# Kernel tuning notes

Hardware: AMD Instinct MI355X
Metric: run time of the kernel (lower is better)

Reference implementation:

```python
import jax, jax.numpy as jnp
import numpy as np
from jax import lax

_CLIP_MIN = 1e-06
_CLIP_MAX = 1.0
_POS_ALPHA = 0.0005
NUM_CLASSES = 21
RADIUS = 3
HALF_D = RADIUS * RADIUS
POOL = 3
PAD = POOL // 2
IGNORE = 255
LAM = 0.5  # loss_weight_lambda, lambda_way=1


def _max_pool(x):
    # NCHW max pool, kernel=stride=3, padding=1
    return lax.reduce_window(x, -jnp.inf, lax.max,
                             (1, 1, POOL, POOL), (1, 1, POOL, POOL),
                             ((0, 0), (0, 0), (PAD, PAD), (PAD, PAD)))


def _get_pairs(x):
    # stack radius*radius shifted crops -> [N, C, r^2, nh, nw]
    h, w = x.shape[2], x.shape[3]
    nh, nw = h - RADIUS + 1, w - RADIUS + 1
    crops = [x[:, :, y:y + nh, xo:xo + nw] for y in range(RADIUS) for xo in range(RADIUS)]
    return jnp.stack(crops, axis=2)


def _log_det_by_cholesky(m):
    chol = jnp.linalg.cholesky(m)
    return 2.0 * jnp.sum(jnp.log(jnp.diagonal(chol, axis1=-2, axis2=-1) + 1e-08), axis=-1)


def _rmi_lower_bound(labels_4d, probs_4d):
    la = _max_pool(labels_4d)
    pr = _max_pool(probs_4d)
    n, c = la.shape[0], la.shape[1]
    la_v = _get_pairs(la).reshape(n, c, HALF_D, -1)   # [N,C,d,L]
    pr_v = _get_pairs(pr).reshape(n, c, HALF_D, -1)
    la_v = la_v - jnp.mean(la_v, axis=3, keepdims=True)
    pr_v = pr_v - jnp.mean(pr_v, axis=3, keepdims=True)
    la_cov = jnp.einsum('ncdl,ncel->ncde', la_v, la_v)
    pr_cov = jnp.einsum('ncdl,ncel->ncde', pr_v, pr_v)
    eye = jnp.eye(HALF_D, dtype=la_cov.dtype)
    pr_cov_inv = jnp.linalg.inv(pr_cov + eye * _POS_ALPHA)
    la_pr_cov = jnp.einsum('ncdl,ncel->ncde', la_v, pr_v)
    appro_var = la_cov - jnp.einsum('ncde,ncef,ncgf->ncdg', la_pr_cov, pr_cov_inv, la_pr_cov)
    rmi_now = 0.5 * _log_det_by_cholesky(appro_var + eye * _POS_ALPHA)  # [N,C]
    rmi_per_class = jnp.mean(rmi_now.reshape(-1, NUM_CLASSES), axis=0) / float(HALF_D)
    return jnp.sum(rmi_per_class)


def setup_inputs() -> dict:
    key = jax.random.key(0)
    k1, k2 = jax.random.split(key)
    score = jax.random.normal(k1, (4, NUM_CLASSES, 512, 512), dtype=jnp.float32)
    target = jax.random.randint(k2, (4, 512, 512), 0, NUM_CLASSES, dtype=jnp.int64)
    return {"score": score, "target": target}


def reference(score, target):
    # cross entropy with ignore_index=255, mean reduction
    logp = jax.nn.log_softmax(score, axis=1)                      # [N,C,H,W]
    valid_ce = (target != IGNORE)
    safe_t = jnp.where(valid_ce, target, 0)
    nll = -jnp.take_along_axis(logp, safe_t[:, None].astype(jnp.int32), axis=1)[:, 0]
    normal_loss = jnp.sum(jnp.where(valid_ce, nll, 0.0)) / jnp.sum(valid_ce.astype(jnp.float32))

    # valid one-hot labels and masked sigmoid probs
    mask = (target < NUM_CLASSES)                                 # [N,H,W]
    maskf = mask.astype(jnp.float32)
    onehot = jax.nn.one_hot((target * mask).astype(jnp.int32), NUM_CLASSES, dtype=jnp.float32)
    onehot = onehot * maskf[..., None]                            # [N,H,W,C]
    onehot = jnp.transpose(onehot, (0, 3, 1, 2))                  # [N,C,H,W]
    probs = jnp.clip(jax.nn.sigmoid(score) * maskf[:, None], _CLIP_MIN, _CLIP_MAX)

    rmi_loss = _rmi_lower_bound(onehot, probs)
    return LAM * normal_loss + rmi_loss * (1.0 - LAM)
```

## Files before the change

kernel.cpp:

```cpp
#include <hip/hip_runtime.h>
#include <cfloat>
#include <cmath>

#define DEVINL __device__ __forceinline__

constexpr int N_ = 4, C_ = 21, H_ = 512, W_ = 512;
constexpr int P_ = 171;
constexpr int Q_ = 169;
constexpr int NC_ = N_ * C_;
constexpr int HW_ = H_ * W_;
constexpr int PP_ = P_ * P_;
constexpr int PROW_ = 172;
constexpr int PPAD_ = PROW_ * P_;
constexpr int NCOV_ = 189;
constexpr float EPS_ = 5e-4f;
constexpr int RC_ = 29;
constexpr int G_ = 43;

DEVINL constexpr int tstart(int d) { return d * 9 - d * (d - 1) / 2; }

DEVINL float wave_sum(float v) {
#pragma unroll
    for (int o = 32; o > 0; o >>= 1) v += __shfl_down(v, o, 64);
    return v;
}

__global__ __launch_bounds__(256) void k_bits(const int* __restrict__ target,
                                              unsigned* __restrict__ pack) {
    int tid = blockIdx.x * 256 + threadIdx.x;
    if (tid >= N_ * PP_) return;
    int cell = tid % PP_;
    int n = tid / PP_;
    int j = cell % P_;
    int i = cell / P_;
    int hl = 3 * i - 1; if (hl < 0) hl = 0;
    int wl = 3 * j - 1; if (wl < 0) wl = 0;
    int hmax = 3 * i + 1, wmax = 3 * j + 1;
    const int* tb = target + (size_t)n * HW_;
    unsigned oh = 0, px = 0;
#pragma unroll
    for (int r = 0; r < 3; ++r) {
        int hh = hl + r;
        bool hv = hh <= hmax;
        const int* trow = tb + hh * W_;
#pragma unroll
        for (int dc = 0; dc < 3; ++dc) {
            int ww = wl + dc;
            int t = trow[ww];
            if (hv && (ww <= wmax) && t >= 0 && t < C_) {
                oh |= 1u << t;
                px |= 1u << (r * 3 + dc);
            }
        }
    }
    pack[tid] = oh | (px << 23);
}

__global__ __launch_bounds__(256) void k_ce(const float* __restrict__ score,
                                            const int* __restrict__ target,
                                            float* __restrict__ cov_ce) {
    int tid = blockIdx.x * 256 + threadIdx.x;
    int p0 = tid * 4;
    int n = p0 >> 18;
    int hw = p0 & (HW_ - 1);
    const float* sp = score + (size_t)n * C_ * HW_ + hw;

    float4 s[C_];
#pragma unroll
    for (int c = 0; c < C_; ++c)
        s[c] = *(const float4*)(sp + (size_t)c * HW_);
    int4 t4 = *(const int4*)(target + p0);

    float4 se = {0.f, 0.f, 0.f, 0.f};
    float4 stgt = {0.f, 0.f, 0.f, 0.f};
#pragma unroll
    for (int c = 0; c < C_; ++c) {
        se.x += __expf(s[c].x);
        se.y += __expf(s[c].y);
        se.z += __expf(s[c].z);
        se.w += __expf(s[c].w);
        if (t4.x == c) stgt.x = s[c].x;
        if (t4.y == c) stgt.y = s[c].y;
        if (t4.z == c) stgt.z = s[c].z;
        if (t4.w == c) stgt.w = s[c].w;
    }
    float nll = 0.f, cnt = 0.f;
    if (t4.x != 255) { nll += __logf(se.x) - stgt.x; cnt += 1.f; }
    if (t4.y != 255) { nll += __logf(se.y) - stgt.y; cnt += 1.f; }
    if (t4.z != 255) { nll += __logf(se.z) - stgt.z; cnt += 1.f; }
    if (t4.w != 255) { nll += __logf(se.w) - stgt.w; cnt += 1.f; }

    nll = wave_sum(nll);
    cnt = wave_sum(cnt);
    __shared__ float rn[4], rc[4];
    int wv = threadIdx.x >> 6, lane = threadIdx.x & 63;
    if (lane == 0) { rn[wv] = nll; rc[wv] = cnt; }
    __syncthreads();
    if (threadIdx.x == 0) {
        atomicAdd(&cov_ce[NC_ * NCOV_ + 0], rn[0] + rn[1] + rn[2] + rn[3]);
        atomicAdd(&cov_ce[NC_ * NCOV_ + 1], rc[0] + rc[1] + rc[2] + rc[3]);
    }
}

template <int IDX>
DEVINL void do_cell(const float (&f)[3][16], unsigned pk, int c, float* prp, float* lap) {
    unsigned px = pk >> 23;
    float vm = -FLT_MAX;
#pragma unroll
    for (int r = 0; r < 3; ++r)
#pragma unroll
        for (int dc = 0; dc < 3; ++dc)
            vm = fmaxf(vm, ((px >> (r * 3 + dc)) & 1u) ? f[r][IDX + dc] : -FLT_MAX);
    float p = __builtin_amdgcn_rcpf(1.f + __expf(-vm));
    p = fminf(fmaxf(p, 1e-6f), 1.f);
    *prp = p;
    *lap = ((pk >> c) & 1u) ? 1.f : 0.f;
}

__global__ __launch_bounds__(256) void k_pool(const float* __restrict__ score,
                                              const unsigned* __restrict__ pack,
                                              float* __restrict__ pr,
                                              float* __restrict__ la) {
    int tid = blockIdx.x * 256 + threadIdx.x;
    if (tid >= NC_ * P_ * G_) return;
    int g = tid % G_;
    int rest = tid / G_;
    int i = rest % P_;
    int ncidx = rest / P_;
    int n = ncidx / C_;
    int c = ncidx - n * C_;

    int hl = 3 * i - 1; if (hl < 0) hl = 0;
    int b = (g == 0) ? 0 : 12 * g - 4;
    int o3 = (b + 15 < W_) ? 12 : 8;

    const float* sb = score + (size_t)ncidx * HW_ + (size_t)hl * W_ + b;
    float f[3][16];
#pragma unroll
    for (int r = 0; r < 3; ++r) {
        const float* rp = sb + r * W_;
        float4 q0 = *(const float4*)(rp);
        float4 q1 = *(const float4*)(rp + 4);
        float4 q2 = *(const float4*)(rp + 8);
        float4 q3 = *(const float4*)(rp + o3);
        f[r][0] = q0.x;  f[r][1] = q0.y;  f[r][2] = q0.z;  f[r][3] = q0.w;
        f[r][4] = q1.x;  f[r][5] = q1.y;  f[r][6] = q1.z;  f[r][7] = q1.w;
        f[r][8] = q2.x;  f[r][9] = q2.y;  f[r][10] = q2.z; f[r][11] = q2.w;
        f[r][12] = q3.x; f[r][13] = q3.y; f[r][14] = q3.z; f[r][15] = q3.w;
    }

    const unsigned* pkp = pack + n * PP_ + i * P_ + 4 * g;
    size_t ob = (size_t)ncidx * PPAD_ + (size_t)i * PROW_ + 4 * g;
    if (g == 0) {
        do_cell<0>(f, pkp[0], c, pr + ob + 0, la + ob + 0);
        do_cell<2>(f, pkp[1], c, pr + ob + 1, la + ob + 1);
        do_cell<5>(f, pkp[2], c, pr + ob + 2, la + ob + 2);
        do_cell<8>(f, pkp[3], c, pr + ob + 3, la + ob + 3);
    } else {
        do_cell<3>(f, pkp[0], c, pr + ob + 0, la + ob + 0);
        do_cell<6>(f, pkp[1], c, pr + ob + 1, la + ob + 1);
        do_cell<9>(f, pkp[2], c, pr + ob + 2, la + ob + 2);
        if (4 * g + 3 < P_)
            do_cell<12>(f, pkp[3], c, pr + ob + 3, la + ob + 3);
    }
}

__global__ __launch_bounds__(256) void k_cov(const float* __restrict__ la,
                                             const float* __restrict__ pr,
                                             float* __restrict__ cov) {
    int nc = blockIdx.x;
    int chunk = blockIdx.y;
    int part = blockIdx.z;
    int r0 = chunk * RC_;
    int rend = r0 + RC_;
    if (rend > Q_) rend = Q_;
    int nitems = (rend - r0) * G_;

    __shared__ float red[4][81];
    int lane = threadIdx.x & 63;
    int wv = threadIdx.x >> 6;

    if (part < 2) {
        const float* X = (part == 0 ? la : pr) + (size_t)nc * PPAD_;
        float s1[9], s2[45];
#pragma unroll
        for (int k = 0; k < 9; ++k) s1[k] = 0.f;
#pragma unroll
        for (int k = 0; k < 45; ++k) s2[k] = 0.f;
        for (int idx = threadIdx.x; idx < nitems; idx += 256) {
            int lr = idx / G_;
            int q = idx - lr * G_;
            int x0 = q * 4;
            const float* base = X + (r0 + lr) * PROW_ + x0;
            float v[3][8];
#pragma unroll
            for (int r = 0; r < 3; ++r) {
                float4 u0 = *(const float4*)(base + r * PROW_);
                float4 u1 = *(const float4*)(base + r * PROW_ + 4);
                v[r][0] = u0.x; v[r][1] = u0.y; v[r][2] = u0.z; v[r][3] = u0.w;
                v[r][4] = u1.x; v[r][5] = u1.y; v[r][6] = u1.z; v[r][7] = u1.w;
            }
#pragma unroll
            for (int p = 0; p < 4; ++p) {
                if (x0 + p < Q_) {
#pragma unroll
                    for (int d = 0; d < 9; ++d) s1[d] += v[d / 3][p + d % 3];
                    int k = 0;
#pragma unroll
                    for (int d = 0; d < 9; ++d)
#pragma unroll
                        for (int e = d; e < 9; ++e) {
                            s2[k] += v[d / 3][p + d % 3] * v[e / 3][p + e % 3];
                            ++k;
                        }
                }
            }
        }
#pragma unroll
        for (int k = 0; k < 9; ++k) { float v2 = wave_sum(s1[k]); if (lane == 0) red[wv][k] = v2; }
#pragma unroll
        for (int k = 0; k < 45; ++k) { float v2 = wave_sum(s2[k]); if (lane == 0) red[wv][9 + k] = v2; }
        __syncthreads();
        int b1 = (part == 0) ? 0 : 9;
        int b2 = (part == 0) ? 18 : 63;
        for (int k = threadIdx.x; k < 54; k += 256) {
            float v2 = red[0][k] + red[1][k] + red[2][k] + red[3][k];
            int dst = (k < 9) ? (b1 + k) : (b2 + k - 9);
            atomicAdd(&cov[nc * NCOV_ + dst], v2);
        }
    } else {
        const float* A = la + (size_t)nc * PPAD_;
        const float* B = pr + (size_t)nc * PPAD_;
        float sab[81];
#pragma unroll
        for (int k = 0; k < 81; ++k) sab[k] = 0.f;
        for (int idx = threadIdx.x; idx < nitems; idx += 256) {
            int lr = idx / G_;
            int q = idx - lr * G_;
            int x0 = q * 4;
            size_t off = (size_t)(r0 + lr) * PROW_ + x0;
            float a[3][8], b[3][8];
#pragma unroll
            for (int r = 0; r < 3; ++r) {
                float4 u0 = *(const float4*)(A + off + r * PROW_);
                float4 u1 = *(const float4*)(A + off + r * PROW_ + 4);
                a[r][0] = u0.x; a[r][1] = u0.y; a[r][2] = u0.z; a[r][3] = u0.w;
                a[r][4] = u1.x; a[r][5] = u1.y; a[r][6] = u1.z; a[r][7] = u1.w;
                float4 w0 = *(const float4*)(B + off + r * PROW_);
                float4 w1 = *(const float4*)(B + off + r * PROW_ + 4);
                b[r][0] = w0.x; b[r][1] = w0.y; b[r][2] = w0.z; b[r][3] = w0.w;
                b[r][4] = w1.x; b[r][5] = w1.y; b[r][6] = w1.z; b[r][7] = w1.w;
            }
#pragma unroll
            for (int p = 0; p < 4; ++p) {
                if (x0 + p < Q_) {
#pragma unroll
                    for (int d = 0; d < 9; ++d)
#pragma unroll
                        for (int e = 0; e < 9; ++e)
                            sab[d * 9 + e] += a[d / 3][p + d % 3] * b[e / 3][p + e % 3];
                }
            }
        }
#pragma unroll
        for (int k = 0; k < 81; ++k) { float v2 = wave_sum(sab[k]); if (lane == 0) red[wv][k] = v2; }
        __syncthreads();
        for (int k = threadIdx.x; k < 81; k += 256) {
            float v2 = red[0][k] + red[1][k] + red[2][k] + red[3][k];
            atomicAdd(&cov[nc * NCOV_ + 108 + k], v2);
        }
    }
}

__global__ __launch_bounds__(128) void k_final(const float* __restrict__ cov,
                                               float* __restrict__ out) {
    __shared__ float red[128];
    int t = threadIdx.x;
    float my = 0.f;
    if (t < NC_) {
        const float* S = cov + t * NCOV_;
        const float Lf = (float)(Q_ * Q_);
        float sA[9], sB[9];
#pragma unroll
        for (int d = 0; d < 9; ++d) { sA[d] = S[d]; sB[d] = S[9 + d]; }
        float laC[45], M[45], Cm[81];
        {
            int k = 0;
#pragma unroll
            for (int d = 0; d < 9; ++d)
#pragma unroll
                for (int e = d; e < 9; ++e) {
                    laC[k] = S[18 + k] - sA[d] * sA[e] / Lf;
                    M[k] = S[63 + k] - sB[d] * sB[e] / Lf + (d == e ? EPS_ : 0.f);
                    ++k;
                }
#pragma unroll
            for (int d = 0; d < 9; ++d)
#pragma unroll
                for (int e = 0; e < 9; ++e)
                    Cm[d * 9 + e] = S[108 + d * 9 + e] - sA[d] * sB[e] / Lf;
        }
#pragma unroll
        for (int j = 0; j < 9; ++j) {
            float s = M[tstart(j)];
#pragma unroll
            for (int k = 0; k < j; ++k) { float l = M[tstart(k) + (j - k)]; s -= l * l; }
            float dj = sqrtf(fmaxf(s, 1e-30f));
            M[tstart(j)] = dj;
            float inv = 1.f / dj;
#pragma unroll
            for (int i = j + 1; i < 9; ++i) {
                float s2 = M[tstart(j) + (i - j)];
#pragma unroll
                for (int k = 0; k < j; ++k)
                    s2 -= M[tstart(k) + (i - k)] * M[tstart(k) + (j - k)];
                M[tstart(j) + (i - j)] = s2 * inv;
            }
        }
#pragma unroll
        for (int p = 0; p < 9; ++p) {
#pragma unroll
            for (int i = 0; i < 9; ++i) {
                float s = Cm[p * 9 + i];
#pragma unroll
                for (int k = 0; k < i; ++k)
                    s -= M[tstart(k) + (i - k)] * Cm[p * 9 + k];
                Cm[p * 9 + i] = s / M[tstart(i)];
            }
        }
#pragma unroll
        for (int d = 0; d < 9; ++d)
#pragma unroll
            for (int e = d; e < 9; ++e) {
                float s = 0.f;
#pragma unroll
                for (int i = 0; i < 9; ++i) s += Cm[d * 9 + i] * Cm[e * 9 + i];
                laC[tstart(d) + (e - d)] -= s;
                if (d == e) laC[tstart(d)] += EPS_;
            }
        float rmi = 0.f;
#pragma unroll
        for (int j = 0; j < 9; ++j) {
            float s = laC[tstart(j)];
#pragma unroll
            for (int k = 0; k < j; ++k) { float l = laC[tstart(k) + (j - k)]; s -= l * l; }
            float dj = sqrtf(fmaxf(s, 0.f));
            laC[tstart(j)] = dj;
            float inv = 1.f / fmaxf(dj, 1e-30f);
#pragma unroll
            for (int i = j + 1; i < 9; ++i) {
                float s2 = laC[tstart(j) + (i - j)];
#pragma unroll
                for (int k = 0; k < j; ++k)
                    s2 -= laC[tstart(k) + (i - k)] * laC[tstart(k) + (j - k)];
                laC[tstart(j) + (i - j)] = s2 * inv;
            }
            rmi += __logf(dj + 1e-8f);
        }
        my = rmi;
    }
    red[t] = my;
    __syncthreads();
#pragma unroll
    for (int o = 64; o > 0; o >>= 1) {
        if (t < o) red[t] += red[t + o];
        __syncthreads();
    }
    if (t == 0) {
        float rmi_total = red[0] / 36.f;
        float ce = cov[NC_ * NCOV_ + 0] / cov[NC_ * NCOV_ + 1];
        out[0] = 0.5f * ce + 0.5f * rmi_total;
    }
}

extern "C" void kernel_launch(void* const* d_in, const int* in_sizes, int n_in,
                              void* d_out, int out_size, void* d_ws, size_t ws_size,
                              hipStream_t stream) {
    const float* score = (const float*)d_in[0];
    const int* target = (const int*)d_in[1];
    float* pr = (float*)d_ws;
    float* la = pr + (size_t)NC_ * PPAD_;
    float* cov = la + (size_t)NC_ * PPAD_;
    unsigned* pack = (unsigned*)(cov + NC_ * NCOV_ + 2);
    hipMemsetAsync(cov, 0, (size_t)(NC_ * NCOV_ + 2) * sizeof(float), stream);

    k_bits<<<dim3((N_ * PP_ + 255) / 256), dim3(256), 0, stream>>>(target, pack);
    k_ce<<<dim3(N_ * HW_ / 4 / 256), dim3(256), 0, stream>>>(score, target, cov);
    k_pool<<<dim3((NC_ * P_ * G_ + 255) / 256), dim3(256), 0, stream>>>(score, pack, pr, la);
    k_cov<<<dim3(NC_, 6, 3), dim3(256), 0, stream>>>(la, pr, cov);
    k_final<<<dim3(1), dim3(128), 0, stream>>>(cov, (float*)d_out);
}
```

Measured before the change: 254.1 us.

## Stage covariance tiles in LDS and split moment terms across waves

The covariance kernel now copies the la and pr row chunks for each (nc, chunk) into shared memory once. Eight waves then each compute a disjoint subset of the self and cross moment terms from LDS, instead of three separate blocks each rereading global memory. Every wave reduces its own accumulators with wave shuffles and issues atomics directly, so the block-level shared reduction is gone. In exchange the grid has fewer blocks, the load is uneven across waves, each wave issues more atomics, and 512-thread blocks use large LDS.

```diff
diff --git a/kernel.cpp b/kernel.cpp
--- a/kernel.cpp
+++ b/kernel.cpp
@@ -9,13 +9,14 @@
 constexpr int Q_ = 169;
 constexpr int NC_ = N_ * C_;
 constexpr int HW_ = H_ * W_;
-constexpr int PP_ = P_ * P_;
+constexpr int PP_ = 29241;
 constexpr int PROW_ = 172;
 constexpr int PPAD_ = PROW_ * P_;
 constexpr int NCOV_ = 189;
 constexpr float EPS_ = 5e-4f;
 constexpr int RC_ = 29;
 constexpr int G_ = 43;
+constexpr int SROW_ = 176;
 
 DEVINL constexpr int tstart(int d) { return d * 9 - d * (d - 1) / 2; }
 
@@ -165,110 +166,141 @@
     }
 }
 
-__global__ __launch_bounds__(256) void k_cov(const float* __restrict__ la,
+template <int D0, int D1, bool S1, int S1B, int S2B>
+DEVINL void tri_lds(const float (*X)[SROW_], int nq, int lane,
+                    float* __restrict__ cov, int nc) {
+    constexpr int NP = ((9 - D0) * (10 - D0) - (9 - D1) * (10 - D1)) / 2;
+    constexpr int NS = S1 ? 9 : 0;
+    constexpr int RLO = D0 / 3;
+    float acc[NS + NP];
+#pragma unroll
+    for (int k = 0; k < NS + NP; ++k) acc[k] = 0.f;
+
+    for (int qi = lane; qi < nq; qi += 64) {
+        int lr = qi / G_;
+        int q = qi - lr * G_;
+        int x0 = 4 * q;
+        float v[3][8];
+#pragma unroll
+        for (int r = RLO; r < 3; ++r) {
+            float4 u0 = *(const float4*)&X[lr + r][x0];
+            float4 u1 = *(const float4*)&X[lr + r][x0 + 4];
+            v[r][0] = u0.x; v[r][1] = u0.y; v[r][2] = u0.z; v[r][3] = u0.w;
+            v[r][4] = u1.x; v[r][5] = u1.y; v[r][6] = u1.z; v[r][7] = u1.w;
+        }
+#pragma unroll
+        for (int p = 0; p < 4; ++p) {
+            if (x0 + p < Q_) {
+                if constexpr (S1) {
+#pragma unroll
+                    for (int d = 0; d < 9; ++d) acc[d] += v[d / 3][p + d % 3];
+                }
+                int k = NS;
+#pragma unroll
+                for (int d = D0; d < D1; ++d)
+#pragma unroll
+                    for (int e = d; e < 9; ++e) {
+                        acc[k] += v[d / 3][p + d % 3] * v[e / 3][p + e % 3];
+                        ++k;
+                    }
+            }
+        }
+    }
+#pragma unroll
+    for (int k = 0; k < NS + NP; ++k) {
+        float v2 = wave_sum(acc[k]);
+        if (lane == 0) {
+            int dst = (S1 && k < 9) ? (S1B + k) : (S2B + tstart(D0) + k - NS);
+            atomicAdd(&cov[nc * NCOV_ + dst], v2);
+        }
+    }
+}
+
+template <int R0, int R1>
+DEVINL void ab_lds(const float (*LA)[SROW_], const float (*PR)[SROW_],
+                   int nq, int lane, float* __restrict__ cov, int nc) {
+    constexpr int NA = (R1 - R0) * 9;
+    constexpr int ALO = R0 / 3, AHI = (R1 - 1) / 3;
+    float acc[NA];
+#pragma unroll
+    for (int k = 0; k < NA; ++k) acc[k] = 0.f;
+
+    for (int qi = lane; qi < nq; qi += 64) {
+        int lr = qi / G_;
+        int q = qi - lr * G_;
+        int x0 = 4 * q;
+        float av[3][8], bv[3][8];
+#pragma unroll
+        for (int r = ALO; r <= AHI; ++r) {
+            float4 u0 = *(const float4*)&LA[lr + r][x0];
+            float4 u1 = *(const float4*)&LA[lr + r][x0 + 4];
+            av[r][0] = u0.x; av[r][1] = u0.y; av[r][2] = u0.z; av[r][3] = u0.w;
+            av[r][4] = u1.x; av[r][5] = u1.y; av[r][6] = u1.z; av[r][7] = u1.w;
+        }
+#pragma unroll
+        for (int r = 0; r < 3; ++r) {
+            float4 u0 = *(const float4*)&PR[lr + r][x0];
+            float4 u1 = *(const float4*)&PR[lr + r][x0 + 4];
+            bv[r][0] = u0.x; bv[r][1] = u0.y; bv[r][2] = u0.z; bv[r][3] = u0.w;
+            bv[r][4] = u1.x; bv[r][5] = u1.y; bv[r][6] = u1.z; bv[r][7] = u1.w;
+        }
+#pragma unroll
+        for (int p = 0; p < 4; ++p) {
+            if (x0 + p < Q_) {
+#pragma unroll
+                for (int d = R0; d < R1; ++d)
+#pragma unroll
+                    for (int e = 0; e < 9; ++e)
+                        acc[(d - R0) * 9 + e] += av[d / 3][p + d % 3] * bv[e / 3][p + e % 3];
+            }
+        }
+    }
+#pragma unroll
+    for (int k = 0; k < NA; ++k) {
+        float v2 = wave_sum(acc[k]);
+        if (lane == 0)
+            atomicAdd(&cov[nc * NCOV_ + 108 + R0 * 9 + k], v2);
+    }
+}
+
+__global__ __launch_bounds__(512) void k_cov(const float* __restrict__ la,
                                              const float* __restrict__ pr,
                                              float* __restrict__ cov) {
+    __shared__ float sLA[31][SROW_];
+    __shared__ float sPR[31][SROW_];
     int nc = blockIdx.x;
     int chunk = blockIdx.y;
-    int part = blockIdx.z;
     int r0 = chunk * RC_;
     int rend = r0 + RC_;
     if (rend > Q_) rend = Q_;
-    int nitems = (rend - r0) * G_;
-
-    __shared__ float red[4][81];
+    int nrows = rend - r0 + 2;
+    int nq = (rend - r0) * G_;
+
+    const float* LAg = la + (size_t)nc * PPAD_;
+    const float* PRg = pr + (size_t)nc * PPAD_;
+    for (int idx = threadIdx.x; idx < nrows * G_; idx += 512) {
+        int rr = idx / G_;
+        int cc = (idx - rr * G_) * 4;
+        *(float4*)&sLA[rr][cc] = *(const float4*)(LAg + (size_t)(r0 + rr) * PROW_ + cc);
+        *(float4*)&sPR[rr][cc] = *(const float4*)(PRg + (size_t)(r0 + rr) * PROW_ + cc);
+    }
+    __syncthreads();
+
+    int wv = threadIdx.x >> 6;
     int lane = threadIdx.x & 63;
-    int wv = threadIdx.x >> 6;
-
-    if (part < 2) {
-        const float* X = (part == 0 ? la : pr) + (size_t)nc * PPAD_;
-        float s1[9], s2[45];
-#pragma unroll
-        for (int k = 0; k < 9; ++k) s1[k] = 0.f;
-#pragma unroll
-        for (int k = 0; k < 45; ++k) s2[k] = 0.f;
-        for (int idx = threadIdx.x; idx < nitems; idx += 256) {
-            int lr = idx / G_;
-            int q = idx - lr * G_;
-            int x0 = q * 4;
-            const float* base = X + (r0 + lr) * PROW_ + x0;
-            float v[3][8];
-#pragma unroll
-            for (int r = 0; r < 3; ++r) {
-                float4 u0 = *(const float4*)(base + r * PROW_);
-                float4 u1 = *(const float4*)(base + r * PROW_ + 4);
-                v[r][0] = u0.x; v[r][1] = u0.y; v[r][2] = u0.z; v[r][3] = u0.w;
-                v[r][4] = u1.x; v[r][5] = u1.y; v[r][6] = u1.z; v[r][7] = u1.w;
-            }
-#pragma unroll
-            for (int p = 0; p < 4; ++p) {
-                if (x0 + p < Q_) {
-#pragma unroll
-                    for (int d = 0; d < 9; ++d) s1[d] += v[d / 3][p + d % 3];
-                    int k = 0;
-#pragma unroll
-                    for (int d = 0; d < 9; ++d)
-#pragma unroll
-                        for (int e = d; e < 9; ++e) {
-                            s2[k] += v[d / 3][p + d % 3] * v[e / 3][p + e % 3];
-                            ++k;
-                        }
-                }
-            }
-        }
-#pragma unroll
-        for (int k = 0; k < 9; ++k) { float v2 = wave_sum(s1[k]); if (lane == 0) red[wv][k] = v2; }
-#pragma unroll
-        for (int k = 0; k < 45; ++k) { float v2 = wave_sum(s2[k]); if (lane == 0) red[wv][9 + k] = v2; }
-        __syncthreads();
-        int b1 = (part == 0) ? 0 : 9;
-        int b2 = (part == 0) ? 18 : 63;
-        for (int k = threadIdx.x; k < 54; k += 256) {
-            float v2 = red[0][k] + red[1][k] + red[2][k] + red[3][k];
-            int dst = (k < 9) ? (b1 + k) : (b2 + k - 9);
-            atomicAdd(&cov[nc * NCOV_ + dst], v2);
-        }
-    } else {
-        const float* A = la + (size_t)nc * PPAD_;
-        const float* B = pr + (size_t)nc * PPAD_;
-        float sab[81];
-#pragma unroll
-        for (int k = 0; k < 81; ++k) sab[k] = 0.f;
-        for (int idx = threadIdx.x; idx < nitems; idx += 256) {
-            int lr = idx / G_;
-            int q = idx - lr * G_;
-            int x0 = q * 4;
-            size_t off = (size_t)(r0 + lr) * PROW_ + x0;
-            float a[3][8], b[3][8];
-#pragma unroll
-            for (int r = 0; r < 3; ++r) {
-                float4 u0 = *(const float4*)(A + off + r * PROW_);
-                float4 u1 = *(const float4*)(A + off + r * PROW_ + 4);
-                a[r][0] = u0.x; a[r][1] = u0.y; a[r][2] = u0.z; a[r][3] = u0.w;
-                a[r][4] = u1.x; a[r][5] = u1.y; a[r][6] = u1.z; a[r][7] = u1.w;
-                float4 w0 = *(const float4*)(B + off + r * PROW_);
-                float4 w1 = *(const float4*)(B + off + r * PROW_ + 4);
-                b[r][0] = w0.x; b[r][1] = w0.y; b[r][2] = w0.z; b[r][3] = w0.w;
-                b[r][4] = w1.x; b[r][5] = w1.y; b[r][6] = w1.z; b[r][7] = w1.w;
-            }
-#pragma unroll
-            for (int p = 0; p < 4; ++p) {
-                if (x0 + p < Q_) {
-#pragma unroll
-                    for (int d = 0; d < 9; ++d)
-#pragma unroll
-                        for (int e = 0; e < 9; ++e)
-                            sab[d * 9 + e] += a[d / 3][p + d % 3] * b[e / 3][p + e % 3];
-                }
-            }
-        }
-#pragma unroll
-        for (int k = 0; k < 81; ++k) { float v2 = wave_sum(sab[k]); if (lane == 0) red[wv][k] = v2; }
-        __syncthreads();
-        for (int k = threadIdx.x; k < 81; k += 256) {
-            float v2 = red[0][k] + red[1][k] + red[2][k] + red[3][k];
-            atomicAdd(&cov[nc * NCOV_ + 108 + k], v2);
-        }
+    switch (wv) {
+        case 0: tri_lds<0, 2, true, 0, 18>(sLA, nq, lane, cov, nc); break;
+        case 1: tri_lds<2, 5, false, 0, 18>(sLA, nq, lane, cov, nc);
+                ab_lds<8, 9>(sLA, sPR, nq, lane, cov, nc); break;
+        case 2: tri_lds<5, 9, false, 0, 18>(sLA, nq, lane, cov, nc);
+                ab_lds<7, 8>(sLA, sPR, nq, lane, cov, nc); break;
+        case 3: tri_lds<0, 2, true, 9, 63>(sPR, nq, lane, cov, nc); break;
+        case 4: tri_lds<2, 5, false, 9, 63>(sPR, nq, lane, cov, nc);
+                ab_lds<6, 7>(sLA, sPR, nq, lane, cov, nc); break;
+        case 5: tri_lds<5, 9, false, 9, 63>(sPR, nq, lane, cov, nc);
+                ab_lds<5, 6>(sLA, sPR, nq, lane, cov, nc); break;
+        case 6: ab_lds<0, 3>(sLA, sPR, nq, lane, cov, nc); break;
+        case 7: ab_lds<3, 5>(sLA, sPR, nq, lane, cov, nc); break;
     }
 }
 
@@ -387,6 +419,6 @@
     k_bits<<<dim3((N_ * PP_ + 255) / 256), dim3(256), 0, stream>>>(target, pack);
     k_ce<<<dim3(N_ * HW_ / 4 / 256), dim3(256), 0, stream>>>(score, target, cov);
     k_pool<<<dim3((NC_ * P_ * G_ + 255) / 256), dim3(256), 0, stream>>>(score, pack, pr, la);
-    k_cov<<<dim3(NC_, 6, 3), dim3(256), 0, stream>>>(la, pr, cov);
+    k_cov<<<dim3(NC_, 6), dim3(512), 0, stream>>>(la, pr, cov);
     k_final<<<dim3(1), dim3(128), 0, stream>>>(cov, (float*)d_out);
 }
```

After: 257.4 us. No clear change (+1.3%).

## Split covariance kernel into per-part kernels with row-offset cross blocks

Applied to the files above, without the earlier changes.

Replaces the single three-part covariance kernel with two launches of a triangular self-covariance kernel and a cross-covariance kernel split over the three row offsets. The cross kernel now keeps 27 accumulators per block instead of 81, which cuts register pressure. Rows are split into 13 chunks of 13 instead of 6 of 29 to expose more blocks. Row padding grows to 176 and the pool kernel zero-fills the tail columns, so the boundary branch is replaced by a multiply mask. The cost is more launches, extra atomics and some redundant loads.

```diff
diff --git a/kernel.cpp b/kernel.cpp
--- a/kernel.cpp
+++ b/kernel.cpp
@@ -9,12 +9,13 @@
 constexpr int Q_ = 169;
 constexpr int NC_ = N_ * C_;
 constexpr int HW_ = H_ * W_;
-constexpr int PP_ = P_ * P_;
-constexpr int PROW_ = 172;
+constexpr int PP_ = 29241;
+constexpr int PROW_ = 176;
 constexpr int PPAD_ = PROW_ * P_;
 constexpr int NCOV_ = 189;
 constexpr float EPS_ = 5e-4f;
-constexpr int RC_ = 29;
+constexpr int RC_ = 13;
+constexpr int NCH_ = 13;
 constexpr int G_ = 43;
 
 DEVINL constexpr int tstart(int d) { return d * 9 - d * (d - 1) / 2; }
@@ -160,115 +161,129 @@
         do_cell<3>(f, pkp[0], c, pr + ob + 0, la + ob + 0);
         do_cell<6>(f, pkp[1], c, pr + ob + 1, la + ob + 1);
         do_cell<9>(f, pkp[2], c, pr + ob + 2, la + ob + 2);
-        if (4 * g + 3 < P_)
+        if (g < G_ - 1)
             do_cell<12>(f, pkp[3], c, pr + ob + 3, la + ob + 3);
-    }
-}
-
-__global__ __launch_bounds__(256) void k_cov(const float* __restrict__ la,
-                                             const float* __restrict__ pr,
-                                             float* __restrict__ cov) {
+        else {
+#pragma unroll
+            for (int z = 3; z < 8; ++z) { pr[ob + z] = 0.f; la[ob + z] = 0.f; }
+        }
+    }
+}
+
+__global__ __launch_bounds__(256, 1) void k_cov_tri(const float* __restrict__ xg,
+                                                    float* __restrict__ cov,
+                                                    int s1base, int s2base) {
     int nc = blockIdx.x;
-    int chunk = blockIdx.y;
-    int part = blockIdx.z;
-    int r0 = chunk * RC_;
-    int rend = r0 + RC_;
-    if (rend > Q_) rend = Q_;
-    int nitems = (rend - r0) * G_;
-
-    __shared__ float red[4][81];
-    int lane = threadIdx.x & 63;
-    int wv = threadIdx.x >> 6;
-
-    if (part < 2) {
-        const float* X = (part == 0 ? la : pr) + (size_t)nc * PPAD_;
-        float s1[9], s2[45];
-#pragma unroll
-        for (int k = 0; k < 9; ++k) s1[k] = 0.f;
-#pragma unroll
-        for (int k = 0; k < 45; ++k) s2[k] = 0.f;
-        for (int idx = threadIdx.x; idx < nitems; idx += 256) {
-            int lr = idx / G_;
-            int q = idx - lr * G_;
-            int x0 = q * 4;
-            const float* base = X + (r0 + lr) * PROW_ + x0;
-            float v[3][8];
-#pragma unroll
-            for (int r = 0; r < 3; ++r) {
-                float4 u0 = *(const float4*)(base + r * PROW_);
-                float4 u1 = *(const float4*)(base + r * PROW_ + 4);
-                v[r][0] = u0.x; v[r][1] = u0.y; v[r][2] = u0.z; v[r][3] = u0.w;
-                v[r][4] = u1.x; v[r][5] = u1.y; v[r][6] = u1.z; v[r][7] = u1.w;
-            }
-#pragma unroll
-            for (int p = 0; p < 4; ++p) {
-                if (x0 + p < Q_) {
-#pragma unroll
-                    for (int d = 0; d < 9; ++d) s1[d] += v[d / 3][p + d % 3];
-                    int k = 0;
-#pragma unroll
-                    for (int d = 0; d < 9; ++d)
-#pragma unroll
-                        for (int e = d; e < 9; ++e) {
-                            s2[k] += v[d / 3][p + d % 3] * v[e / 3][p + e % 3];
-                            ++k;
-                        }
+    int r0 = blockIdx.y * RC_;
+    const float* X = xg + (size_t)nc * PPAD_ + (size_t)r0 * PROW_;
+
+    float s1[9], s2[45];
+#pragma unroll
+    for (int k = 0; k < 9; ++k) s1[k] = 0.f;
+#pragma unroll
+    for (int k = 0; k < 45; ++k) s2[k] = 0.f;
+
+    for (int qi = threadIdx.x; qi < RC_ * G_; qi += 256) {
+        int lr = qi / G_;
+        int q = qi - lr * G_;
+        int x0 = 4 * q;
+        const float* base = X + lr * PROW_ + x0;
+        float v[3][8];
+#pragma unroll
+        for (int r = 0; r < 3; ++r) {
+            float4 u0 = *(const float4*)(base + r * PROW_);
+            float4 u1 = *(const float4*)(base + r * PROW_ + 4);
+            v[r][0] = u0.x; v[r][1] = u0.y; v[r][2] = u0.z; v[r][3] = u0.w;
+            v[r][4] = u1.x; v[r][5] = u1.y; v[r][6] = u1.z; v[r][7] = u1.w;
+        }
+#pragma unroll
+        for (int p = 0; p < 4; ++p) {
+            float mp = (x0 + p < Q_) ? 1.f : 0.f;
+            float w[9];
+#pragma unroll
+            for (int d = 0; d < 9; ++d) w[d] = v[d / 3][p + d % 3] * mp;
+#pragma unroll
+            for (int d = 0; d < 9; ++d) s1[d] += w[d];
+            int k = 0;
+#pragma unroll
+            for (int d = 0; d < 9; ++d)
+#pragma unroll
+                for (int e = d; e < 9; ++e) {
+                    s2[k] += w[d] * v[e / 3][p + e % 3];
+                    ++k;
                 }
-            }
-        }
-#pragma unroll
-        for (int k = 0; k < 9; ++k) { float v2 = wave_sum(s1[k]); if (lane == 0) red[wv][k] = v2; }
-#pragma unroll
-        for (int k = 0; k < 45; ++k) { float v2 = wave_sum(s2[k]); if (lane == 0) red[wv][9 + k] = v2; }
-        __syncthreads();
-        int b1 = (part == 0) ? 0 : 9;
-        int b2 = (part == 0) ? 18 : 63;
-        for (int k = threadIdx.x; k < 54; k += 256) {
-            float v2 = red[0][k] + red[1][k] + red[2][k] + red[3][k];
-            int dst = (k < 9) ? (b1 + k) : (b2 + k - 9);
-            atomicAdd(&cov[nc * NCOV_ + dst], v2);
-        }
-    } else {
-        const float* A = la + (size_t)nc * PPAD_;
-        const float* B = pr + (size_t)nc * PPAD_;
-        float sab[81];
-#pragma unroll
-        for (int k = 0; k < 81; ++k) sab[k] = 0.f;
-        for (int idx = threadIdx.x; idx < nitems; idx += 256) {
-            int lr = idx / G_;
-            int q = idx - lr * G_;
-            int x0 = q * 4;
-            size_t off = (size_t)(r0 + lr) * PROW_ + x0;
-            float a[3][8], b[3][8];
-#pragma unroll
-            for (int r = 0; r < 3; ++r) {
-                float4 u0 = *(const float4*)(A + off + r * PROW_);
-                float4 u1 = *(const float4*)(A + off + r * PROW_ + 4);
-                a[r][0] = u0.x; a[r][1] = u0.y; a[r][2] = u0.z; a[r][3] = u0.w;
-                a[r][4] = u1.x; a[r][5] = u1.y; a[r][6] = u1.z; a[r][7] = u1.w;
-                float4 w0 = *(const float4*)(B + off + r * PROW_);
-                float4 w1 = *(const float4*)(B + off + r * PROW_ + 4);
-                b[r][0] = w0.x; b[r][1] = w0.y; b[r][2] = w0.z; b[r][3] = w0.w;
-                b[r][4] = w1.x; b[r][5] = w1.y; b[r][6] = w1.z; b[r][7] = w1.w;
-            }
-#pragma unroll
-            for (int p = 0; p < 4; ++p) {
-                if (x0 + p < Q_) {
-#pragma unroll
-                    for (int d = 0; d < 9; ++d)
-#pragma unroll
-                        for (int e = 0; e < 9; ++e)
-                            sab[d * 9 + e] += a[d / 3][p + d % 3] * b[e / 3][p + e % 3];
-                }
-            }
-        }
-#pragma unroll
-        for (int k = 0; k < 81; ++k) { float v2 = wave_sum(sab[k]); if (lane == 0) red[wv][k] = v2; }
-        __syncthreads();
-        for (int k = threadIdx.x; k < 81; k += 256) {
-            float v2 = red[0][k] + red[1][k] + red[2][k] + red[3][k];
-            atomicAdd(&cov[nc * NCOV_ + 108 + k], v2);
-        }
+        }
+    }
+
+    __shared__ float red[4][54];
+    int lane = threadIdx.x & 63, wv = threadIdx.x >> 6;
+#pragma unroll
+    for (int k = 0; k < 9; ++k) { float v2 = wave_sum(s1[k]); if (lane == 0) red[wv][k] = v2; }
+#pragma unroll
+    for (int k = 0; k < 45; ++k) { float v2 = wave_sum(s2[k]); if (lane == 0) red[wv][9 + k] = v2; }
+    __syncthreads();
+    for (int k = threadIdx.x; k < 54; k += 256) {
+        float v2 = red[0][k] + red[1][k] + red[2][k] + red[3][k];
+        int dst = (k < 9) ? (s1base + k) : (s2base + k - 9);
+        atomicAdd(&cov[nc * NCOV_ + dst], v2);
+    }
+}
+
+__global__ __launch_bounds__(256, 1) void k_cov_ab(const float* __restrict__ la,
+                                                   const float* __restrict__ pr,
+                                                   float* __restrict__ cov) {
+    int nc = blockIdx.x;
+    int r0 = blockIdx.y * RC_;
+    int RA = blockIdx.z;
+    const float* A = la + (size_t)nc * PPAD_ + (size_t)r0 * PROW_;
+    const float* B = pr + (size_t)nc * PPAD_ + (size_t)r0 * PROW_;
+
+    float acc[27];
+#pragma unroll
+    for (int k = 0; k < 27; ++k) acc[k] = 0.f;
+
+    for (int qi = threadIdx.x; qi < RC_ * G_; qi += 256) {
+        int lr = qi / G_;
+        int q = qi - lr * G_;
+        int x0 = 4 * q;
+        const float* ap = A + (lr + RA) * PROW_ + x0;
+        const float* bp = B + lr * PROW_ + x0;
+        float a[8], b[3][8];
+        {
+            float4 u0 = *(const float4*)(ap);
+            float4 u1 = *(const float4*)(ap + 4);
+            a[0] = u0.x; a[1] = u0.y; a[2] = u0.z; a[3] = u0.w;
+            a[4] = u1.x; a[5] = u1.y; a[6] = u1.z; a[7] = u1.w;
+        }
+#pragma unroll
+        for (int r = 0; r < 3; ++r) {
+            float4 u0 = *(const float4*)(bp + r * PROW_);
+            float4 u1 = *(const float4*)(bp + r * PROW_ + 4);
+            b[r][0] = u0.x; b[r][1] = u0.y; b[r][2] = u0.z; b[r][3] = u0.w;
+            b[r][4] = u1.x; b[r][5] = u1.y; b[r][6] = u1.z; b[r][7] = u1.w;
+        }
+#pragma unroll
+        for (int p = 0; p < 4; ++p) {
+            float mp = (x0 + p < Q_) ? 1.f : 0.f;
+            float am[3];
+#pragma unroll
+            for (int c1 = 0; c1 < 3; ++c1) am[c1] = a[p + c1] * mp;
+#pragma unroll
+            for (int c1 = 0; c1 < 3; ++c1)
+#pragma unroll
+                for (int e = 0; e < 9; ++e)
+                    acc[c1 * 9 + e] += am[c1] * b[e / 3][p + e % 3];
+        }
+    }
+
+    __shared__ float red[4][27];
+    int lane = threadIdx.x & 63, wv = threadIdx.x >> 6;
+#pragma unroll
+    for (int k = 0; k < 27; ++k) { float v2 = wave_sum(acc[k]); if (lane == 0) red[wv][k] = v2; }
+    __syncthreads();
+    for (int k = threadIdx.x; k < 27; k += 256) {
+        float v2 = red[0][k] + red[1][k] + red[2][k] + red[3][k];
+        atomicAdd(&cov[nc * NCOV_ + 108 + RA * 27 + k], v2);
     }
 }
 
@@ -387,6 +402,8 @@
     k_bits<<<dim3((N_ * PP_ + 255) / 256), dim3(256), 0, stream>>>(target, pack);
     k_ce<<<dim3(N_ * HW_ / 4 / 256), dim3(256), 0, stream>>>(score, target, cov);
     k_pool<<<dim3((NC_ * P_ * G_ + 255) / 256), dim3(256), 0, stream>>>(score, pack, pr, la);
-    k_cov<<<dim3(NC_, 6, 3), dim3(256), 0, stream>>>(la, pr, cov);
+    k_cov_tri<<<dim3(NC_, NCH_), dim3(256), 0, stream>>>(la, cov, 0, 18);
+    k_cov_tri<<<dim3(NC_, NCH_), dim3(256), 0, stream>>>(pr, cov, 9, 63);
+    k_cov_ab<<<dim3(NC_, NCH_, 3), dim3(256), 0, stream>>>(la, pr, cov);
     k_final<<<dim3(1), dim3(128), 0, stream>>>(cov, (float*)d_out);
 }
```

Result: slower. 302.1 us (+18.9%).
